# Kernel optimization log

Hardware: AMD Instinct MI355X
Metric: run time of the kernel (lower is better)

## Reference

```python
import jax, jax.numpy as jnp
import numpy as np

PATCH = 3
ALPHA = 0.1


def _unfold3x3(x):
    # x: [B, C, H, W] -> [B, C*9, H, W], torch F.unfold with k=3, pad=1, stride=1
    B, C, H, W = x.shape
    p = PATCH // 2
    xp = jnp.pad(x, ((0, 0), (0, 0), (p, p), (p, p)))
    shifts = [xp[:, :, i:i + H, j:j + W] for i in range(PATCH) for j in range(PATCH)]
    # torch unfold orders (C, kh, kw); ordering is irrelevant for the dot-product
    # correlation, but we match it anyway: stack kernel positions after channel.
    out = jnp.stack(shifts, axis=2)  # [B, C, 9, H, W]
    return out.reshape(B, C * PATCH * PATCH, H, W)


def setup_inputs() -> dict:
    key = jax.random.key(0)
    k1, k2 = jax.random.split(key)
    x_lab = jax.random.normal(k1, (4, 3, 64, 64), dtype=jnp.float32)
    feature = jax.random.normal(k2, (4, 64, 64, 64), dtype=jnp.float32)
    return {"x_lab": x_lab, "feature": feature}


def reference(x_lab, feature):
    # scale_factor=1 and feature already at (H, W): both interpolates are identity.
    B, _, H, W = x_lab.shape
    N = H * W
    x_ab = x_lab.reshape(B, 3, N).transpose(0, 2, 1)          # [B, N, 3]
    lf = _unfold3x3(feature).reshape(B, -1, N)                 # [B, C*9, N]
    corr = jnp.einsum('bcn,bcm->bnm', lf, lf)                  # [B, N, N]
    attn = jax.nn.softmax(corr / ALPHA, axis=-1)
    weighted = jnp.einsum('bnm,bmc->bnc', attn, x_ab)          # [B, N, 3]
    return weighted.transpose(0, 2, 1).reshape(B, 3, H, W)
```

## Files before the change

kernel.cpp:

```cpp
#include <hip/hip_runtime.h>
#include <math.h>


#define HH 64
#define WW 64
#define CH 64
#define NPIX 4096
#define SCALE 10.0f
#define ROWCH 528
#define ROWB  (ROWCH * 16)

typedef __attribute__((ext_vector_type(8))) short bf16x8;
typedef __attribute__((ext_vector_type(4))) float f32x4;

__global__ __launch_bounds__(256) void nlwa_pre(const float* __restrict__ f,
                                                uint4* __restrict__ fTg) {
    const int b = blockIdx.x >> 6, y = blockIdx.x & 63;
    const float* fb = f + (size_t)b * CH * NPIX + y * WW;
    uint4* dst = fTg + (size_t)blockIdx.x * ROWCH;
    for (int idx = threadIdx.x; idx < ROWCH; idx += 256) {
        const int kc = idx / 66, xs = idx - kc * 66;
        uint4 v = {0u, 0u, 0u, 0u};
        if (xs >= 1 && xs <= 64) {
            const int x = xs - 1;
            unsigned h[8];
#pragma unroll
            for (int j = 0; j < 8; ++j) {
                unsigned u = __float_as_uint(fb[(size_t)(kc * 8 + j) * NPIX + x]);
                u = u + 0x7fffu + ((u >> 16) & 1u);
                h[j] = u >> 16;
            }
            v.x = h[0] | (h[1] << 16); v.y = h[2] | (h[3] << 16);
            v.z = h[4] | (h[5] << 16); v.w = h[6] | (h[7] << 16);
        }
        dst[idx] = v;
    }
}

__device__ __forceinline__ void gld16(const uint4* g, char* l) {
    __builtin_amdgcn_global_load_lds(
        (const __attribute__((address_space(1))) unsigned int*)g,
        (__attribute__((address_space(3))) unsigned int*)l, 16, 0, 0);
}

__global__ __launch_bounds__(256, 2) void nlwa_main(const float* __restrict__ x_lab,
                                                    const uint4* __restrict__ fTg,
                                                    float* __restrict__ pw) {
    __shared__ __align__(16) char smem[8 * ROWB];

    const int tid = threadIdx.x;
    const int bid = blockIdx.x;
    const int b = bid >> 7, ny = (bid >> 1) & 63, half = bid & 1;
    const int my0 = half * 32;
    const int w = tid >> 6, lane = tid & 63;
    const int quad = lane >> 4, nl = lane & 15;
    const int qofs = (w & 1) * 32;
    const int kofs = (w >> 1) * 32;

    const uint4* fT = fTg + (size_t)b * (64 * ROWCH);

    {
        const uint4 z = {0u, 0u, 0u, 0u};
        uint4* zr = (uint4*)(smem + 7 * ROWB);
        for (int i = tid; i < ROWCH; i += 256) zr[i] = z;
#pragma unroll
        for (int dyi = 0; dyi < 3; ++dyi) {
            const int qr = ny + dyi - 1;
            uint4* dst = (uint4*)(smem + dyi * ROWB);
            if (qr >= 0 && qr < 64) {
                const uint4* src = fT + (size_t)qr * ROWCH;
                for (int i = tid; i < ROWCH; i += 256) dst[i] = src[i];
            } else {
                for (int i = tid; i < ROWCH; i += 256) dst[i] = z;
            }
        }
        for (int r = my0 - 1; r <= my0 + 1; ++r) {
            if (r >= 0 && r < 64) {
                uint4* dst = (uint4*)(smem + (3 + (r & 3)) * ROWB);
                const uint4* src = fT + (size_t)r * ROWCH;
                for (int i = tid; i < ROWCH; i += 256) dst[i] = src[i];
            }
        }
    }
    __syncthreads();

    bf16x8 AF[36];
    const int laneoff = (quad * 66 + nl) * 16;
    {
#pragma unroll
        for (int d = 0; d < 9; ++d) {
            const int dyi = d / 3, dx = d - dyi * 3;
#pragma unroll
            for (int ks = 0; ks < 2; ++ks) {
#pragma unroll
                for (int ti = 0; ti < 2; ++ti) {
                    const int off = dyi * ROWB + laneoff +
                                    (ks * 264 + qofs + ti * 16 + dx) * 16;
                    AF[(d * 2 + ks) * 2 + ti] = *(const bf16x8*)(smem + off);
                }
            }
        }
    }

    float m_[8], l_[8], A0[8], A1[8], A2[8];
#pragma unroll
    for (int s = 0; s < 8; ++s) {
        m_[s] = -3.0e38f; l_[s] = 0.0f; A0[s] = 0.0f; A1[s] = 0.0f; A2[s] = 0.0f;
    }

    const float* xl = x_lab + (size_t)b * 3 * NPIX;
    const int kx0 = kofs + nl, kx1 = kofs + 16 + nl;

    for (int my = my0; my < my0 + 32; ++my) {
        {
            int pr = my + 2; if (pr > 63) pr = 63;
            const uint4* src = fT + (size_t)pr * ROWCH + w * 132 + lane;
            char* dst = smem + (3 + ((my + 2) & 3)) * ROWB + w * 132 * 16;
            gld16(src, dst);
            gld16(src + 64, dst + 1024);
            if (lane < 4) gld16(src + 128, dst + 2048);
        }
        const float* xr = xl + my * 64;
        const float xv00 = xr[kx0], xv01 = xr[NPIX + kx0], xv02 = xr[2 * NPIX + kx0];
        const float xv10 = xr[kx1], xv11 = xr[NPIX + kx1], xv12 = xr[2 * NPIX + kx1];

        const char* kb[3];
#pragma unroll
        for (int dyi = 0; dyi < 3; ++dyi) {
            const int kr = my + dyi - 1;
            kb[dyi] = (kr >= 0 && kr < 64) ? (smem + (3 + (kr & 3)) * ROWB)
                                           : (smem + 7 * ROWB);
        }

        f32x4 a00 = {0.f, 0.f, 0.f, 0.f}, a01 = a00, a10 = a00, a11 = a00;
#pragma unroll
        for (int d = 0; d < 9; ++d) {
            const char* base = kb[d / 3];
            const int dx = d - (d / 3) * 3;
#pragma unroll
            for (int ks = 0; ks < 2; ++ks) {
                const int uo = (ks * 264 + kofs + dx) * 16;
                const bf16x8 B0 = *(const bf16x8*)(base + laneoff + uo);
                const bf16x8 B1 = *(const bf16x8*)(base + laneoff + uo + 256);
                const int fi = (d * 2 + ks) * 2;
                a00 = __builtin_amdgcn_mfma_f32_16x16x32_bf16(AF[fi + 0], B0, a00, 0, 0, 0);
                a10 = __builtin_amdgcn_mfma_f32_16x16x32_bf16(AF[fi + 1], B0, a10, 0, 0, 0);
                a01 = __builtin_amdgcn_mfma_f32_16x16x32_bf16(AF[fi + 0], B1, a01, 0, 0, 0);
                a11 = __builtin_amdgcn_mfma_f32_16x16x32_bf16(AF[fi + 1], B1, a11, 0, 0, 0);
            }
        }

#pragma unroll
        for (int ti = 0; ti < 2; ++ti) {
#pragma unroll
            for (int r = 0; r < 4; ++r) {
                const int s = ti * 4 + r;
                const float v0 = (ti ? a10[r] : a00[r]) * SCALE;
                const float v1 = (ti ? a11[r] : a01[r]) * SCALE;
                const float mn = fmaxf(m_[s], fmaxf(v0, v1));
                const float sc = __expf(m_[s] - mn);
                const float e0 = __expf(v0 - mn);
                const float e1 = __expf(v1 - mn);
                l_[s] = l_[s] * sc + e0 + e1;
                A0[s] = A0[s] * sc + e0 * xv00 + e1 * xv10;
                A1[s] = A1[s] * sc + e0 * xv01 + e1 * xv11;
                A2[s] = A2[s] * sc + e0 * xv02 + e1 * xv12;
                m_[s] = mn;
            }
        }
        __syncthreads();
    }

    float* scr = (float*)smem;
    const int p = (w >> 1) * 16 + nl;
#pragma unroll
    for (int s = 0; s < 8; ++s) {
        const int q = qofs + (s >> 2) * 16 + quad * 4 + (s & 3);
        float* o = scr + (q * 32 + p) * 5;
        o[0] = m_[s]; o[1] = l_[s]; o[2] = A0[s]; o[3] = A1[s]; o[4] = A2[s];
    }
    __syncthreads();
    if (tid < 64) {
        const float* basep = scr + tid * 32 * 5;
        float mx = -3.0e38f;
        for (int i = 0; i < 32; ++i) mx = fmaxf(mx, basep[i * 5]);
        float L = 0.f, c0 = 0.f, c1 = 0.f, c2 = 0.f;
        for (int i = 0; i < 32; ++i) {
            const float* pp = basep + i * 5;
            const float wgt = __expf(pp[0] - mx);
            L += wgt * pp[1]; c0 += wgt * pp[2]; c1 += wgt * pp[3]; c2 += wgt * pp[4];
        }
        float* o = pw + (size_t)bid * 512 + tid * 8;
        o[0] = mx; o[1] = L; o[2] = c0; o[3] = c1; o[4] = c2;
    }
}

__global__ __launch_bounds__(64) void nlwa_combine(const float* __restrict__ pw,
                                                   float* __restrict__ out) {
    const int r = blockIdx.x;
    const int q = threadIdx.x;
    const float* p0 = pw + (size_t)(r * 2) * 512 + q * 8;
    const float* p1 = p0 + 512;
    const float m0 = p0[0], m1 = p1[0];
    const float mx = fmaxf(m0, m1);
    const float w0 = __expf(m0 - mx), w1 = __expf(m1 - mx);
    const float L = w0 * p0[1] + w1 * p1[1];
    const float inv = 1.0f / L;
    const int b = r >> 6, ny = r & 63;
    float* o = out + (size_t)b * 3 * NPIX + ny * 64 + q;
    o[0]        = (w0 * p0[2] + w1 * p1[2]) * inv;
    o[NPIX]     = (w0 * p0[3] + w1 * p1[3]) * inv;
    o[2 * NPIX] = (w0 * p0[4] + w1 * p1[4]) * inv;
}

extern "C" void kernel_launch(void* const* d_in, const int* in_sizes, int n_in,
                              void* d_out, int out_size, void* d_ws, size_t ws_size,
                              hipStream_t stream) {
    (void)in_sizes; (void)n_in; (void)out_size; (void)ws_size;
    const float* x_lab   = (const float*)d_in[0];
    const float* feature = (const float*)d_in[1];
    float* out = (float*)d_out;
    uint4* fTg = (uint4*)d_ws;
    float* pw  = (float*)((char*)d_ws + (size_t)256 * ROWB);
    nlwa_pre<<<dim3(256), dim3(256), 0, stream>>>(feature, fTg);
    nlwa_main<<<dim3(512), dim3(256), 0, stream>>>(x_lab, fTg, pw);
    nlwa_combine<<<dim3(256), dim3(64), 0, stream>>>(pw, out);
}
```

Measured before the change: 138.4 us.

## Split key rows across warp pairs in-block, fuse combine into main kernel

The main kernel now uses 512-thread blocks, one per query row. The two halves of the block take alternating key rows over all 64 key rows, so the split-key partial softmax states are merged in LDS instead of through a separate combine kernel and global scratch. Query fragments are loaded straight from global memory, and a 6-slot ring buffer of key rows replaces the old 4-slot scheme. This removes one kernel launch and the partial-result round trip to global memory. The cost is 256 blocks instead of 512, which may reduce occupancy and overlap on the device.

After: 135.5 us. 1.02x faster.

```diff
diff --git a/kernel.cpp b/kernel.cpp
--- a/kernel.cpp
+++ b/kernel.cpp
@@ -1,5 +1,4 @@
 #include <hip/hip_runtime.h>
-#include <math.h>
 
 
 #define HH 64
@@ -43,60 +42,48 @@
         (__attribute__((address_space(3))) unsigned int*)l, 16, 0, 0);
 }
 
-__global__ __launch_bounds__(256, 2) void nlwa_main(const float* __restrict__ x_lab,
+__global__ __launch_bounds__(512, 2) void nlwa_main(const float* __restrict__ x_lab,
                                                     const uint4* __restrict__ fTg,
-                                                    float* __restrict__ pw) {
-    __shared__ __align__(16) char smem[8 * ROWB];
+                                                    float* __restrict__ out) {
+    __shared__ __align__(16) char smem[7 * ROWB];
 
     const int tid = threadIdx.x;
-    const int bid = blockIdx.x;
-    const int b = bid >> 7, ny = (bid >> 1) & 63, half = bid & 1;
-    const int my0 = half * 32;
+    const int b = blockIdx.x >> 6, ny = blockIdx.x & 63;
     const int w = tid >> 6, lane = tid & 63;
     const int quad = lane >> 4, nl = lane & 15;
-    const int qofs = (w & 1) * 32;
-    const int kofs = (w >> 1) * 32;
+    const int qhalf = w & 1, khalf = (w >> 1) & 1, par = w >> 2;
+    const int qofs = qhalf * 32, kofs = khalf * 32;
 
     const uint4* fT = fTg + (size_t)b * (64 * ROWCH);
 
     {
         const uint4 z = {0u, 0u, 0u, 0u};
-        uint4* zr = (uint4*)(smem + 7 * ROWB);
-        for (int i = tid; i < ROWCH; i += 256) zr[i] = z;
-#pragma unroll
-        for (int dyi = 0; dyi < 3; ++dyi) {
-            const int qr = ny + dyi - 1;
-            uint4* dst = (uint4*)(smem + dyi * ROWB);
-            if (qr >= 0 && qr < 64) {
-                const uint4* src = fT + (size_t)qr * ROWCH;
-                for (int i = tid; i < ROWCH; i += 256) dst[i] = src[i];
-            } else {
-                for (int i = tid; i < ROWCH; i += 256) dst[i] = z;
-            }
-        }
-        for (int r = my0 - 1; r <= my0 + 1; ++r) {
-            if (r >= 0 && r < 64) {
-                uint4* dst = (uint4*)(smem + (3 + (r & 3)) * ROWB);
-                const uint4* src = fT + (size_t)r * ROWCH;
-                for (int i = tid; i < ROWCH; i += 256) dst[i] = src[i];
-            }
-        }
-    }
-    __syncthreads();
+        uint4* s6 = (uint4*)(smem + 6 * ROWB);
+        for (int i = tid; i < ROWCH; i += 512) s6[i] = z;
+#pragma unroll
+        for (int r = 0; r < 3; ++r) {
+            uint4* dst = (uint4*)(smem + r * ROWB);
+            const uint4* src = fT + (size_t)r * ROWCH;
+            for (int i = tid; i < ROWCH; i += 512) dst[i] = src[i];
+        }
+    }
 
     bf16x8 AF[36];
-    const int laneoff = (quad * 66 + nl) * 16;
     {
+        const bf16x8 zf = {0, 0, 0, 0, 0, 0, 0, 0};
 #pragma unroll
         for (int d = 0; d < 9; ++d) {
             const int dyi = d / 3, dx = d - dyi * 3;
+            const int qr = ny + dyi - 1;
+            const bool ok = (qr >= 0) && (qr < 64);
+            const char* rowp = (const char*)(fT + (size_t)(ok ? qr : 0) * ROWCH);
 #pragma unroll
             for (int ks = 0; ks < 2; ++ks) {
 #pragma unroll
                 for (int ti = 0; ti < 2; ++ti) {
-                    const int off = dyi * ROWB + laneoff +
-                                    (ks * 264 + qofs + ti * 16 + dx) * 16;
-                    AF[(d * 2 + ks) * 2 + ti] = *(const bf16x8*)(smem + off);
+                    const int unit = (quad + ks * 4) * 66 + (qofs + ti * 16 + nl + dx);
+                    AF[(d * 2 + ks) * 2 + ti] =
+                        ok ? *(const bf16x8*)(rowp + unit * 16) : zf;
                 }
             }
         }
@@ -110,26 +97,41 @@
 
     const float* xl = x_lab + (size_t)b * 3 * NPIX;
     const int kx0 = kofs + nl, kx1 = kofs + 16 + nl;
-
-    for (int my = my0; my < my0 + 32; ++my) {
+    const int laneoff = (quad * 66 + nl) * 16;
+
+    __syncthreads();
+
+    for (int my2 = 0; my2 < 64; my2 += 2) {
+        const int myw = my2 + par;
+
         {
-            int pr = my + 2; if (pr > 63) pr = 63;
-            const uint4* src = fT + (size_t)pr * ROWCH + w * 132 + lane;
-            char* dst = smem + (3 + ((my + 2) & 3)) * ROWB + w * 132 * 16;
-            gld16(src, dst);
-            gld16(src + 64, dst + 1024);
-            if (lane < 4) gld16(src + 128, dst + 2048);
-        }
-        const float* xr = xl + my * 64;
+            const int pr = my2 + 3 + par;
+            if (pr <= 63) {
+                const uint4* src = fT + (size_t)pr * ROWCH;
+                char* dst = smem + (pr % 6) * ROWB;
+                const int seg = w & 3;
+#pragma unroll
+                for (int j = 0; j < 2; ++j) {
+                    const int u = (seg * 2 + j) * 64 + lane;
+                    gld16(src + u, dst + u * 16);
+                }
+                if ((w & 3) == 0 && lane < 16) {
+                    const int u = 512 + lane;
+                    gld16(src + u, dst + u * 16);
+                }
+            }
+        }
+
+        const float* xr = xl + myw * 64;
         const float xv00 = xr[kx0], xv01 = xr[NPIX + kx0], xv02 = xr[2 * NPIX + kx0];
         const float xv10 = xr[kx1], xv11 = xr[NPIX + kx1], xv12 = xr[2 * NPIX + kx1];
 
         const char* kb[3];
 #pragma unroll
         for (int dyi = 0; dyi < 3; ++dyi) {
-            const int kr = my + dyi - 1;
-            kb[dyi] = (kr >= 0 && kr < 64) ? (smem + (3 + (kr & 3)) * ROWB)
-                                           : (smem + 7 * ROWB);
+            const int kr = myw + dyi - 1;
+            kb[dyi] = (kr >= 0 && kr < 64) ? (smem + (kr % 6) * ROWB)
+                                           : (smem + 6 * ROWB);
         }
 
         f32x4 a00 = {0.f, 0.f, 0.f, 0.f}, a01 = a00, a10 = a00, a11 = a00;
@@ -172,12 +174,30 @@
     }
 
     float* scr = (float*)smem;
-    const int p = (w >> 1) * 16 + nl;
-#pragma unroll
-    for (int s = 0; s < 8; ++s) {
-        const int q = qofs + (s >> 2) * 16 + quad * 4 + (s & 3);
-        float* o = scr + (q * 32 + p) * 5;
-        o[0] = m_[s]; o[1] = l_[s]; o[2] = A0[s]; o[3] = A1[s]; o[4] = A2[s];
+    const int p = khalf * 16 + nl;
+    if (par == 0) {
+#pragma unroll
+        for (int s = 0; s < 8; ++s) {
+            const int q = qofs + (s >> 2) * 16 + quad * 4 + (s & 3);
+            float* o = scr + (q * 32 + p) * 5;
+            o[0] = m_[s]; o[1] = l_[s]; o[2] = A0[s]; o[3] = A1[s]; o[4] = A2[s];
+        }
+    }
+    __syncthreads();
+    if (par == 1) {
+#pragma unroll
+        for (int s = 0; s < 8; ++s) {
+            const int q = qofs + (s >> 2) * 16 + quad * 4 + (s & 3);
+            float* o = scr + (q * 32 + p) * 5;
+            const float m2 = o[0];
+            const float mn = fmaxf(m_[s], m2);
+            const float w1 = __expf(m_[s] - mn), w2 = __expf(m2 - mn);
+            o[0] = mn;
+            o[1] = w1 * l_[s] + w2 * o[1];
+            o[2] = w1 * A0[s] + w2 * o[2];
+            o[3] = w1 * A1[s] + w2 * o[3];
+            o[4] = w1 * A2[s] + w2 * o[4];
+        }
     }
     __syncthreads();
     if (tid < 64) {
@@ -190,27 +210,12 @@
             const float wgt = __expf(pp[0] - mx);
             L += wgt * pp[1]; c0 += wgt * pp[2]; c1 += wgt * pp[3]; c2 += wgt * pp[4];
         }
-        float* o = pw + (size_t)bid * 512 + tid * 8;
-        o[0] = mx; o[1] = L; o[2] = c0; o[3] = c1; o[4] = c2;
-    }
-}
-
-__global__ __launch_bounds__(64) void nlwa_combine(const float* __restrict__ pw,
-                                                   float* __restrict__ out) {
-    const int r = blockIdx.x;
-    const int q = threadIdx.x;
-    const float* p0 = pw + (size_t)(r * 2) * 512 + q * 8;
-    const float* p1 = p0 + 512;
-    const float m0 = p0[0], m1 = p1[0];
-    const float mx = fmaxf(m0, m1);
-    const float w0 = __expf(m0 - mx), w1 = __expf(m1 - mx);
-    const float L = w0 * p0[1] + w1 * p1[1];
-    const float inv = 1.0f / L;
-    const int b = r >> 6, ny = r & 63;
-    float* o = out + (size_t)b * 3 * NPIX + ny * 64 + q;
-    o[0]        = (w0 * p0[2] + w1 * p1[2]) * inv;
-    o[NPIX]     = (w0 * p0[3] + w1 * p1[3]) * inv;
-    o[2 * NPIX] = (w0 * p0[4] + w1 * p1[4]) * inv;
+        const float inv = 1.0f / L;
+        float* o = out + (size_t)b * 3 * NPIX + ny * 64 + tid;
+        o[0]        = c0 * inv;
+        o[NPIX]     = c1 * inv;
+        o[2 * NPIX] = c2 * inv;
+    }
 }
 
 extern "C" void kernel_launch(void* const* d_in, const int* in_sizes, int n_in,
@@ -221,8 +226,6 @@
     const float* feature = (const float*)d_in[1];
     float* out = (float*)d_out;
     uint4* fTg = (uint4*)d_ws;
-    float* pw  = (float*)((char*)d_ws + (size_t)256 * ROWB);
     nlwa_pre<<<dim3(256), dim3(256), 0, stream>>>(feature, fTg);
-    nlwa_main<<<dim3(512), dim3(256), 0, stream>>>(x_lab, fTg, pw);
-    nlwa_combine<<<dim3(256), dim3(64), 0, stream>>>(pw, out);
-}
+    nlwa_main<<<dim3(256), dim3(512), 0, stream>>>(x_lab, fTg, out);
+}
```
